# Performance work log

Hardware: AMD Instinct MI355X
Metric: run time of the kernel (lower is better)

Reference implementation:

```python
import jax, jax.numpy as jnp
import numpy as np

V, E, H, L = 37, 256, 512, 3
B, S = 512, 128


def lstm_layer(x, W_ih, W_hh, b_ih, b_hh):
    # x: [B,S,D_in]; W_ih: [4H,D_in]; W_hh: [4H,H]; PyTorch gate order i,f,g,o
    Bx = x.shape[0]
    Hh = W_hh.shape[1]
    x_proj = jnp.einsum('bsd,gd->bsg', x, W_ih) + b_ih + b_hh  # [B,S,4H]

    def step(carry, xt):
        h, c = carry
        gates = xt + h @ W_hh.T
        i, f, g, o = jnp.split(gates, 4, axis=-1)
        i = jax.nn.sigmoid(i)
        f = jax.nn.sigmoid(f)
        g = jnp.tanh(g)
        o = jax.nn.sigmoid(o)
        c = f * c + i * g
        h = o * jnp.tanh(c)
        return (h, c), h

    init = (jnp.zeros((Bx, Hh), x.dtype), jnp.zeros((Bx, Hh), x.dtype))
    (hT, cT), hs = jax.lax.scan(step, init, jnp.swapaxes(x_proj, 0, 1))
    return jnp.swapaxes(hs, 0, 1), hT, cT


def setup_inputs() -> dict:
    key = jax.random.key(0)
    ks = jax.random.split(key, 16)
    inp = {'tokens': jax.random.randint(ks[0], (B, S), 0, V)}
    inp['embedding'] = jax.random.normal(ks[1], (V, E), jnp.float32) * 0.05
    for l in range(L):
        d_in = E if l == 0 else H
        inp[f'W_ih{l}'] = jax.random.normal(ks[2 + 4 * l], (4 * H, d_in), jnp.float32) * 0.05
        inp[f'W_hh{l}'] = jax.random.normal(ks[3 + 4 * l], (4 * H, H), jnp.float32) * 0.05
        inp[f'b_ih{l}'] = jnp.zeros((4 * H,), jnp.float32)
        inp[f'b_hh{l}'] = jnp.zeros((4 * H,), jnp.float32)
    inp['W_out'] = jax.random.normal(ks[14], (V, H), jnp.float32) * 0.05
    inp['b_out'] = jnp.zeros((V,), jnp.float32)
    return inp


def reference(tokens, embedding, W_ih0, W_hh0, b_ih0, b_hh0,
              W_ih1, W_hh1, b_ih1, b_hh1,
              W_ih2, W_hh2, b_ih2, b_hh2, W_out, b_out):
    x = embedding[tokens]  # [B,S,E]
    hs, cs = [], []
    for (Wi, Wh, bi, bh) in ((W_ih0, W_hh0, b_ih0, b_hh0),
                             (W_ih1, W_hh1, b_ih1, b_hh1),
                             (W_ih2, W_hh2, b_ih2, b_hh2)):
        x, hT, cT = lstm_layer(x, Wi, Wh, bi, bh)
        hs.append(hT)
        cs.append(cT)
    logits = jnp.einsum('bsh,vh->bsv', x, W_out) + b_out  # [B,S,V]
    return logits, jnp.stack(hs), jnp.stack(cs)
```

## Files before the change

kernel.cpp:

```cpp
#include <hip/hip_runtime.h>

typedef __attribute__((ext_vector_type(4))) float f32x4;
typedef __attribute__((ext_vector_type(8))) short bf16x8;

#define DEV __device__ __forceinline__

DEV float b2f(ushort u) { return __uint_as_float(((uint)u) << 16); }
DEV ushort f2b(float f) {
    uint u = __float_as_uint(f);
    return (ushort)((u + 0x7fffu + ((u >> 16) & 1u)) >> 16);
}
DEV float fsig(float x) {
    return __builtin_amdgcn_rcpf(1.f + __builtin_amdgcn_exp2f(-1.4426950408889634f * x));
}
DEV float ftanh(float x) {
    return 1.f - 2.f * __builtin_amdgcn_rcpf(__builtin_amdgcn_exp2f(2.885390081777927f * x) + 1.f);
}
DEV void gload_lds16(const void* g, void* l) {
    __builtin_amdgcn_global_load_lds(
        (const __attribute__((address_space(1))) void*)g,
        (__attribute__((address_space(3))) void*)l, 16, 0, 0);
}
DEV void gload_lds16_l2(const void* g, void* l) {
    __builtin_amdgcn_global_load_lds(
        (const __attribute__((address_space(1))) void*)g,
        (__attribute__((address_space(3))) void*)l, 16, 0, 1);
}
DEV void store_sc_u32(uint* p, uint v) {
    asm volatile("global_store_dword %0, %1, off sc0 sc1" :: "v"(p), "v"(v) : "memory");
}
DEV uint load_sc_u32(const uint* p) {
    uint v;
    asm volatile("global_load_dword %0, %1, off sc0 sc1\n\ts_waitcnt vmcnt(0)"
                 : "=v"(v) : "v"(p) : "memory");
    return v;
}

__global__ void f2b_kernel(const float* __restrict__ s, ushort* __restrict__ d, int n) {
    int i = blockIdx.x * 256 + threadIdx.x;
    if (i < n) d[i] = f2b(s[i]);
}

__global__ void embed_kernel(const int* __restrict__ tok, const float* __restrict__ emb,
                             ushort* __restrict__ x0) {
    int row = blockIdx.x;
    int t = row >> 9, b = row & 511;
    int tk = tok[b * 128 + t];
    x0[(size_t)row * 256 + threadIdx.x] = f2b(emb[(size_t)tk * 256 + threadIdx.x]);
}

__global__ __launch_bounds__(256) void gemm_bias_kernel(
    const ushort* __restrict__ A, const ushort* __restrict__ Bw,
    const float* __restrict__ bias0, const float* __restrict__ bias1,
    ushort* __restrict__ C, int M, int N, int K) {
    __shared__ ushort la[128 * 32];
    __shared__ ushort lb[128 * 32];
    const int tid = threadIdx.x;
    const int wave = tid >> 6, lane = tid & 63;
    const int ntn = N >> 7;
    const int tm = blockIdx.x / ntn, tn = blockIdx.x % ntn;
    const int m0 = tm << 7, n0 = tn << 7;
    const int wm = (wave >> 1) * 64, wn = (wave & 1) * 64;
    f32x4 acc[4][4] = {};
    const int nks = K >> 5;
    const int srow = tid >> 2, scol = (tid & 3) * 8;
    for (int ks = 0; ks < nks; ++ks) {
        const int k0 = ks << 5;
#pragma unroll
        for (int r = 0; r < 2; ++r) {
            gload_lds16(A + (size_t)(m0 + r * 64 + srow) * K + k0 + scol, &la[r * 2048 + wave * 512]);
            gload_lds16(Bw + (size_t)(n0 + r * 64 + srow) * K + k0 + scol, &lb[r * 2048 + wave * 512]);
        }
        __syncthreads();
        bf16x8 af[4], bfr[4];
#pragma unroll
        for (int i = 0; i < 4; ++i)
            af[i] = *(const bf16x8*)&la[(wm + i * 16 + (lane & 15)) * 32 + (lane >> 4) * 8];
#pragma unroll
        for (int i = 0; i < 4; ++i)
            bfr[i] = *(const bf16x8*)&lb[(wn + i * 16 + (lane & 15)) * 32 + (lane >> 4) * 8];
#pragma unroll
        for (int mi = 0; mi < 4; ++mi)
#pragma unroll
            for (int ni = 0; ni < 4; ++ni)
                acc[mi][ni] = __builtin_amdgcn_mfma_f32_16x16x32_bf16(af[mi], bfr[ni], acc[mi][ni], 0, 0, 0);
        __syncthreads();
    }
#pragma unroll
    for (int mi = 0; mi < 4; ++mi) {
        int row = m0 + wm + mi * 16 + ((lane >> 4) << 2);
#pragma unroll
        for (int j = 0; j < 4; ++j) {
#pragma unroll
            for (int ni = 0; ni < 4; ++ni) {
                int col = n0 + wn + ni * 16 + (lane & 15);
                C[(size_t)(row + j) * N + col] = f2b(acc[mi][ni][j] + bias0[col] + bias1[col]);
            }
        }
    }
}

__global__ __launch_bounds__(256) void lstm_chunk_kernel(
    const ushort* __restrict__ xpj,
    const ushort* __restrict__ Whh,
    ushort* __restrict__ hs,
    float* __restrict__ cstate,
    float* __restrict__ hT, float* __restrict__ cT,
    uint* __restrict__ bar,
    int t0) {
    __shared__ ushort hp[64 * 512];
    __shared__ float gbuf[4][64][20];
    const int tid = threadIdx.x;
    const int wave = tid >> 6, lane = tid & 63;
    const int grp = blockIdx.x & 7;
    const int hsl = blockIdx.x >> 3;
    const int b0 = grp << 6, h0 = hsl << 4;
    uint* gflags = bar + grp * 512;
    uint* myflag = gflags + hsl * 16;

    __threadfence();

    bf16x8 Bfr[16];
    const ushort* wb = Whh + ((size_t)(wave * 512 + h0 + (lane & 15))) * 512 + (lane >> 4) * 8;
#pragma unroll
    for (int ks = 0; ks < 16; ++ks) Bfr[ks] = *(const bf16x8*)(wb + ks * 32);

    float creg[4];
#pragma unroll
    for (int i = 0; i < 2; ++i) {
        const int e2 = i * 512 + tid * 2;
        const size_t ci = (size_t)(b0 + (e2 >> 4)) * 512 + h0 + (e2 & 15);
        if (t0 > 0) {
            float2 cv = *(const float2*)&cstate[ci];
            creg[2 * i] = cv.x; creg[2 * i + 1] = cv.y;
        } else {
            creg[2 * i] = 0.f; creg[2 * i + 1] = 0.f;
        }
    }

    uint xqc[8];
#pragma unroll
    for (int i = 0; i < 2; ++i) {
        const int e2 = i * 512 + tid * 2;
        const uint* xb = (const uint*)(xpj + (size_t)(b0 + (e2 >> 4)) * 2048 + h0 + (e2 & 15));
        xqc[i * 4 + 0] = xb[0]; xqc[i * 4 + 1] = xb[256];
        xqc[i * 4 + 2] = xb[512]; xqc[i * 4 + 3] = xb[768];
    }

    for (int tt = 0; tt < 32; ++tt) {
        const int t = t0 + tt;
        if (tt > 0) {
            if (wave == 0) {
                const uint* fp = gflags + ((lane & 31) << 4);
                const uint target = (uint)tt;
                while (!__all(load_sc_u32(fp) >= target)) __builtin_amdgcn_s_sleep(1);
            }
            __syncthreads();
        }
        f32x4 acc[4] = {};
        uint xqn[8];
        if (t > 0) {
            const ushort* hprev = hs + (size_t)(t - 1) * 262144;
#pragma unroll
            for (int rr = 0; rr < 16; ++rr) {
                const int row = rr * 4 + wave;
                gload_lds16_l2(hprev + (size_t)(b0 + row) * 512 + ((lane ^ (row & 7)) * 8),
                               &hp[row * 512]);
            }
            if (tt < 31) {
                const ushort* xt = xpj + (size_t)(tt + 1) * 1048576;
#pragma unroll
                for (int i = 0; i < 2; ++i) {
                    const int e2 = i * 512 + tid * 2;
                    const uint* xb = (const uint*)(xt + (size_t)(b0 + (e2 >> 4)) * 2048 + h0 + (e2 & 15));
                    xqn[i * 4 + 0] = xb[0]; xqn[i * 4 + 1] = xb[256];
                    xqn[i * 4 + 2] = xb[512]; xqn[i * 4 + 3] = xb[768];
                }
            }
            __syncthreads();
#pragma unroll
            for (int ks = 0; ks < 16; ++ks) {
#pragma unroll
                for (int mi = 0; mi < 4; ++mi) {
                    const int row = mi * 16 + (lane & 15);
                    const int c16 = (ks * 4 + (lane >> 4)) ^ (row & 7);
                    bf16x8 af = *(const bf16x8*)&hp[row * 512 + c16 * 8];
                    acc[mi] = __builtin_amdgcn_mfma_f32_16x16x32_bf16(af, Bfr[ks], acc[mi], 0, 0, 0);
                }
            }
        } else if (tt < 31) {
            const ushort* xt = xpj + (size_t)(tt + 1) * 1048576;
#pragma unroll
            for (int i = 0; i < 2; ++i) {
                const int e2 = i * 512 + tid * 2;
                const uint* xb = (const uint*)(xt + (size_t)(b0 + (e2 >> 4)) * 2048 + h0 + (e2 & 15));
                xqn[i * 4 + 0] = xb[0]; xqn[i * 4 + 1] = xb[256];
                xqn[i * 4 + 2] = xb[512]; xqn[i * 4 + 3] = xb[768];
            }
        }
#pragma unroll
        for (int mi = 0; mi < 4; ++mi) {
            const int rloc = mi * 16 + ((lane >> 4) << 2);
#pragma unroll
            for (int j = 0; j < 4; ++j) gbuf[wave][rloc + j][lane & 15] = acc[mi][j];
        }
        __syncthreads();
        ushort* hout = hs + (size_t)t * 262144;
#pragma unroll
        for (int i = 0; i < 2; ++i) {
            const int e2 = i * 512 + tid * 2;
            const int b = e2 >> 4, hh = e2 & 15;
            float2 gI = *(const float2*)&gbuf[0][b][hh];
            float2 gF = *(const float2*)&gbuf[1][b][hh];
            float2 gG = *(const float2*)&gbuf[2][b][hh];
            float2 gO = *(const float2*)&gbuf[3][b][hh];
            float i0 = fsig(gI.x + b2f((ushort)(xqc[i * 4 + 0] & 0xffff)));
            float i1 = fsig(gI.y + b2f((ushort)(xqc[i * 4 + 0] >> 16)));
            float f0 = fsig(gF.x + b2f((ushort)(xqc[i * 4 + 1] & 0xffff)));
            float f1 = fsig(gF.y + b2f((ushort)(xqc[i * 4 + 1] >> 16)));
            float g0 = ftanh(gG.x + b2f((ushort)(xqc[i * 4 + 2] & 0xffff)));
            float g1 = ftanh(gG.y + b2f((ushort)(xqc[i * 4 + 2] >> 16)));
            float o0 = fsig(gO.x + b2f((ushort)(xqc[i * 4 + 3] & 0xffff)));
            float o1 = fsig(gO.y + b2f((ushort)(xqc[i * 4 + 3] >> 16)));
            float c0 = f0 * creg[2 * i] + i0 * g0;
            float c1 = f1 * creg[2 * i + 1] + i1 * g1;
            float h0v = o0 * ftanh(c0);
            float h1v = o1 * ftanh(c1);
            creg[2 * i] = c0; creg[2 * i + 1] = c1;
            const size_t ci = (size_t)(b0 + b) * 512 + h0 + hh;
            store_sc_u32((uint*)(hout + ci), (uint)f2b(h0v) | ((uint)f2b(h1v) << 16));
            if (t == 127) {
                *(float2*)&hT[ci] = make_float2(h0v, h1v);
                *(float2*)&cT[ci] = make_float2(c0, c1);
            }
        }
        if (tt < 31) {
#pragma unroll
            for (int k = 0; k < 8; ++k) xqc[k] = xqn[k];
        }
        if (tt < 31) {
            asm volatile("s_waitcnt vmcnt(0)" ::: "memory");
            __syncthreads();
            if (tid == 0) store_sc_u32(myflag, (uint)(tt + 1));
        }
    }
#pragma unroll
    for (int i = 0; i < 2; ++i) {
        const int e2 = i * 512 + tid * 2;
        const size_t ci = (size_t)(b0 + (e2 >> 4)) * 512 + h0 + (e2 & 15);
        *(float2*)&cstate[ci] = make_float2(creg[2 * i], creg[2 * i + 1]);
    }
}

__global__ __launch_bounds__(256) void outproj_kernel(
    const ushort* __restrict__ hs, const float* __restrict__ Wout,
    const float* __restrict__ bout, float* __restrict__ out) {
    __shared__ ushort lh[32 * 512];
    const int tid = threadIdx.x;
    const size_t r0 = (size_t)blockIdx.x * 32;
    const uint4* gs = (const uint4*)(hs + r0 * 512);
    uint4* ls = (uint4*)lh;
    for (int i = tid; i < 2048; i += 256) ls[i] = gs[i];
    __syncthreads();
    const int rg = tid & 7, vg = tid >> 3;
    float acc[4][2] = {};
    for (int k8 = 0; k8 < 64; ++k8) {
        float hf[4][8];
#pragma unroll
        for (int rr = 0; rr < 4; ++rr) {
            bf16x8 hv = *(const bf16x8*)&lh[(rg * 4 + rr) * 512 + k8 * 8];
#pragma unroll
            for (int j = 0; j < 8; ++j) hf[rr][j] = b2f((ushort)hv[j]);
        }
#pragma unroll
        for (int vi = 0; vi < 2; ++vi) {
            int v = vg + vi * 32;
            if (v < 37) {
                const float* wp = Wout + (size_t)v * 512 + k8 * 8;
                float4 w0 = *(const float4*)wp;
                float4 w1 = *(const float4*)(wp + 4);
                float wv[8] = {w0.x, w0.y, w0.z, w0.w, w1.x, w1.y, w1.z, w1.w};
#pragma unroll
                for (int rr = 0; rr < 4; ++rr) {
                    float s = 0.f;
#pragma unroll
                    for (int j = 0; j < 8; ++j) s += hf[rr][j] * wv[j];
                    acc[rr][vi] += s;
                }
            }
        }
    }
#pragma unroll
    for (int vi = 0; vi < 2; ++vi) {
        int v = vg + vi * 32;
        if (v < 37) {
#pragma unroll
            for (int rr = 0; rr < 4; ++rr) {
                size_t r = r0 + rg * 4 + rr;
                int t = (int)(r >> 9), b = (int)(r & 511);
                out[((size_t)b * 128 + t) * 37 + v] = acc[rr][vi] + bout[v];
            }
        }
    }
}

extern "C" void kernel_launch(void* const* d_in, const int* in_sizes, int n_in,
                              void* d_out, int out_size, void* d_ws, size_t ws_size,
                              hipStream_t stream) {
    (void)in_sizes; (void)n_in; (void)out_size; (void)ws_size;
    const int* tokens = (const int*)d_in[0];
    const float* emb = (const float*)d_in[1];
    const float* Wih_f[3] = {(const float*)d_in[2], (const float*)d_in[6], (const float*)d_in[10]};
    const float* Whh_f[3] = {(const float*)d_in[3], (const float*)d_in[7], (const float*)d_in[11]};
    const float* bih[3] = {(const float*)d_in[4], (const float*)d_in[8], (const float*)d_in[12]};
    const float* bhh[3] = {(const float*)d_in[5], (const float*)d_in[9], (const float*)d_in[13]};
    const float* Wout = (const float*)d_in[14];
    const float* bout = (const float*)d_in[15];
    float* out = (float*)d_out;

    char* ws = (char*)d_ws;
    size_t off = 0;
    auto take = [&](size_t nb) -> void* {
        void* p = ws + off;
        off = (off + nb + 255) & ~(size_t)255;
        return p;
    };
    ushort* x0 = (ushort*)take((size_t)128 * 512 * 256 * 2);
    ushort* hsA = (ushort*)take((size_t)128 * 512 * 512 * 2);
    ushort* hsB = (ushort*)take((size_t)128 * 512 * 512 * 2);
    ushort* xpj = (ushort*)take((size_t)32 * 512 * 2048 * 2);
    float* cst = (float*)take((size_t)512 * 512 * 4);
    ushort* wih[3];
    wih[0] = (ushort*)take((size_t)2048 * 256 * 2);
    wih[1] = (ushort*)take((size_t)2048 * 512 * 2);
    wih[2] = (ushort*)take((size_t)2048 * 512 * 2);
    ushort* whh[3];
    for (int l = 0; l < 3; ++l) whh[l] = (ushort*)take((size_t)2048 * 512 * 2);
    uint* barbase = (uint*)take((size_t)12 * 4096 * 4);

    hipMemsetAsync(barbase, 0, (size_t)12 * 4096 * 4, stream);

    f2b_kernel<<<2048, 256, 0, stream>>>(Wih_f[0], wih[0], 2048 * 256);
    f2b_kernel<<<4096, 256, 0, stream>>>(Wih_f[1], wih[1], 2048 * 512);
    f2b_kernel<<<4096, 256, 0, stream>>>(Wih_f[2], wih[2], 2048 * 512);
    for (int l = 0; l < 3; ++l)
        f2b_kernel<<<4096, 256, 0, stream>>>(Whh_f[l], whh[l], 2048 * 512);

    embed_kernel<<<65536, 256, 0, stream>>>(tokens, emb, x0);

    float* hTbase = out + 2424832;
    float* cTbase = out + 2424832 + 786432;
    const ushort* src = x0;
    ushort* hs_out = hsA;
    for (int l = 0; l < 3; ++l) {
        int K = (l == 0) ? 256 : 512;
        hs_out = (l == 1) ? hsB : hsA;
        for (int ch = 0; ch < 4; ++ch) {
            gemm_bias_kernel<<<2048, 256, 0, stream>>>(
                src + (size_t)ch * 16384 * K, wih[l], bih[l], bhh[l], xpj, 16384, 2048, K);
            lstm_chunk_kernel<<<256, 256, 0, stream>>>(
                xpj, whh[l], hs_out, cst,
                hTbase + (size_t)l * 262144, cTbase + (size_t)l * 262144,
                barbase + (size_t)(l * 4 + ch) * 4096, ch * 32);
        }
        src = hs_out;
    }
    outproj_kernel<<<2048, 256, 0, stream>>>(hs_out, Wout, bout, out);
}
```

Before: 2.559 ms.

## Retile recurrent MFMA as 2x2 wave grid and vectorize embedding gather

Each wave of the LSTM step kernel now covers two batch row-tiles and two gates instead of four row-tiles and one gate. Each A fragment read from LDS is reused by two MFMAs, which halves LDS reads per wave in the serial recurrent loop. The cost is twice as many W_hh B-fragment registers per wave, which raises register pressure. The embedding kernel also becomes a grid-stride loop over a smaller grid and moves 8 elements per thread with 16-byte loads and stores.

Result: slower. 2.721 ms (+6.3%).

```diff
diff --git a/kernel.cpp b/kernel.cpp
--- a/kernel.cpp
+++ b/kernel.cpp
@@ -41,12 +41,24 @@
     if (i < n) d[i] = f2b(s[i]);
 }
 
-__global__ void embed_kernel(const int* __restrict__ tok, const float* __restrict__ emb,
-                             ushort* __restrict__ x0) {
-    int row = blockIdx.x;
-    int t = row >> 9, b = row & 511;
-    int tk = tok[b * 128 + t];
-    x0[(size_t)row * 256 + threadIdx.x] = f2b(emb[(size_t)tk * 256 + threadIdx.x]);
+__global__ __launch_bounds__(256) void embed_kernel(
+    const int* __restrict__ tok, const float* __restrict__ emb, ushort* __restrict__ x0) {
+    const int nthr = gridDim.x * 256;
+    for (int idx = blockIdx.x * 256 + threadIdx.x; idx < 128 * 512 * 32; idx += nthr) {
+        const int row = idx >> 5;
+        const int g8 = idx & 31;
+        const int t = row >> 9, b = row & 511;
+        const int tk = tok[b * 128 + t];
+        const float* ep = emb + (size_t)tk * 256 + g8 * 8;
+        float4 a = *(const float4*)ep;
+        float4 c = *(const float4*)(ep + 4);
+        uint4 o;
+        o.x = (uint)f2b(a.x) | ((uint)f2b(a.y) << 16);
+        o.y = (uint)f2b(a.z) | ((uint)f2b(a.w) << 16);
+        o.z = (uint)f2b(c.x) | ((uint)f2b(c.y) << 16);
+        o.w = (uint)f2b(c.z) | ((uint)f2b(c.w) << 16);
+        *(uint4*)(x0 + (size_t)row * 256 + g8 * 8) = o;
+    }
 }
 
 __global__ __launch_bounds__(256) void gemm_bias_kernel(
@@ -112,6 +124,8 @@
     __shared__ float gbuf[4][64][20];
     const int tid = threadIdx.x;
     const int wave = tid >> 6, lane = tid & 63;
+    const int l15 = lane & 15, lh = lane >> 4;
+    const int wr = wave >> 1, wc = wave & 1;
     const int grp = blockIdx.x & 7;
     const int hsl = blockIdx.x >> 3;
     const int b0 = grp << 6, h0 = hsl << 4;
@@ -120,10 +134,13 @@
 
     __threadfence();
 
-    bf16x8 Bfr[16];
-    const ushort* wb = Whh + ((size_t)(wave * 512 + h0 + (lane & 15))) * 512 + (lane >> 4) * 8;
-#pragma unroll
-    for (int ks = 0; ks < 16; ++ks) Bfr[ks] = *(const bf16x8*)(wb + ks * 32);
+    bf16x8 Bfr[2][16];
+#pragma unroll
+    for (int gg = 0; gg < 2; ++gg) {
+        const ushort* wb = Whh + (size_t)((2 * wc + gg) * 512 + h0 + l15) * 512 + lh * 8;
+#pragma unroll
+        for (int ks = 0; ks < 16; ++ks) Bfr[gg][ks] = *(const bf16x8*)(wb + ks * 32);
+    }
 
     float creg[4];
 #pragma unroll
@@ -157,7 +174,7 @@
             }
             __syncthreads();
         }
-        f32x4 acc[4] = {};
+        f32x4 acc[2][2] = {};
         uint xqn[8];
         if (t > 0) {
             const ushort* hprev = hs + (size_t)(t - 1) * 262144;
@@ -181,11 +198,12 @@
 #pragma unroll
             for (int ks = 0; ks < 16; ++ks) {
 #pragma unroll
-                for (int mi = 0; mi < 4; ++mi) {
-                    const int row = mi * 16 + (lane & 15);
-                    const int c16 = (ks * 4 + (lane >> 4)) ^ (row & 7);
+                for (int m = 0; m < 2; ++m) {
+                    const int row = (2 * wr + m) * 16 + l15;
+                    const int c16 = (ks * 4 + lh) ^ (row & 7);
                     bf16x8 af = *(const bf16x8*)&hp[row * 512 + c16 * 8];
-                    acc[mi] = __builtin_amdgcn_mfma_f32_16x16x32_bf16(af, Bfr[ks], acc[mi], 0, 0, 0);
+                    acc[m][0] = __builtin_amdgcn_mfma_f32_16x16x32_bf16(af, Bfr[0][ks], acc[m][0], 0, 0, 0);
+                    acc[m][1] = __builtin_amdgcn_mfma_f32_16x16x32_bf16(af, Bfr[1][ks], acc[m][1], 0, 0, 0);
                 }
             }
         } else if (tt < 31) {
@@ -199,11 +217,12 @@
             }
         }
 #pragma unroll
-        for (int mi = 0; mi < 4; ++mi) {
-            const int rloc = mi * 16 + ((lane >> 4) << 2);
-#pragma unroll
-            for (int j = 0; j < 4; ++j) gbuf[wave][rloc + j][lane & 15] = acc[mi][j];
-        }
+        for (int m = 0; m < 2; ++m)
+#pragma unroll
+            for (int gg = 0; gg < 2; ++gg)
+#pragma unroll
+                for (int j = 0; j < 4; ++j)
+                    gbuf[2 * wc + gg][(2 * wr + m) * 16 + lh * 4 + j][l15] = acc[m][gg][j];
         __syncthreads();
         ushort* hout = hs + (size_t)t * 262144;
 #pragma unroll
@@ -346,7 +365,7 @@
     for (int l = 0; l < 3; ++l)
         f2b_kernel<<<4096, 256, 0, stream>>>(Whh_f[l], whh[l], 2048 * 512);
 
-    embed_kernel<<<65536, 256, 0, stream>>>(tokens, emb, x0);
+    embed_kernel<<<2048, 256, 0, stream>>>(tokens, emb, x0);
 
     float* hTbase = out + 2424832;
     float* cTbase = out + 2424832 + 786432;
```
